# Kernel tuning notes

Hardware: AMD Instinct MI355X
Metric: run time of the kernel (lower is better)

Reference implementation:

```python
import jax, jax.numpy as jnp
import numpy as np

# DeepSeek-V2 router config
T = 8192          # tokens (batch*seq)
H = 5120          # hidden_size / gating_dim
E = 160           # n_routed_experts
N_GROUP = 8       # n_group
TOPK_GROUP = 3    # topk_group
TOP_K = 6         # num_experts_per_tok
SCALE = 16.0      # routed_scaling_factor (norm_topk_prob=False path)


def setup_inputs() -> dict:
    key = jax.random.key(0)
    k1, k2 = jax.random.split(key)
    hidden_states = jax.random.normal(k1, (T, H), dtype=jnp.float32)
    # kaiming_uniform init for the gating kernel
    bound = float(np.sqrt(6.0 / H))
    kernel = jax.random.uniform(k2, (E, H), dtype=jnp.float32, minval=-bound, maxval=bound)
    return {"hidden_states": hidden_states, "kernel": kernel}


def reference(hidden_states, kernel):
    # gating matmul in fp32: [T, H] @ [H, E] -> [T, E]
    logits = jnp.einsum("th,eh->te", hidden_states.astype(jnp.float32), kernel.astype(jnp.float32))
    scores = jax.nn.softmax(logits, axis=-1)  # [T, E]

    n_tok = scores.shape[0]
    # group-limited greedy: max score per group -> [T, N_GROUP]
    group_scores = scores.reshape(n_tok, N_GROUP, E // N_GROUP).max(axis=-1)
    top_group_idx = jax.lax.top_k(group_scores, TOPK_GROUP)[1]  # [T, TOPK_GROUP]

    # scatter 1s into selected groups
    row_idx = jnp.arange(n_tok)[:, None]
    group_mask = jnp.zeros_like(group_scores).at[row_idx, top_group_idx].set(1.0)  # [T, N_GROUP]

    # broadcast group mask over experts within each group -> [T, E]
    score_mask = jnp.repeat(group_mask[:, :, None], E // N_GROUP, axis=2).reshape(n_tok, -1)
    masked_scores = jnp.where(score_mask, scores, 0.0)

    topk_weight, _ = jax.lax.top_k(masked_scores, TOP_K)  # [T, TOP_K]
    # norm_topk_prob is False in DeepSeek-V2 -> scale by routed_scaling_factor
    return topk_weight * SCALE
```

## Files before the change

### kernel.cpp

```cpp
#include <hip/hip_runtime.h>
#include <math.h>

#define TT 8192
#define HH 5120
#define EE 160
#define NGRP 8
#define GSZ 20
#define TOPKG 3
#define TOPK 6
#define RSCALE 16.0f
#define SK 8
#define KS (HH / SK)
#define NSG (KS / 32)
#define BMG 256

typedef __attribute__((ext_vector_type(8))) short bf16x8;
typedef __attribute__((ext_vector_type(8))) _Float16 f16x8;
typedef __attribute__((ext_vector_type(4))) float f32x4;

#define BW_ELEMS ((size_t)160 * 10 * 64 * 8)
#define BWH_BYTES (BW_ELEMS * 2)

__device__ __forceinline__ ushort f2bf(float f) {
    uint32_t u = __float_as_uint(f);
    u += 0x7fff + ((u >> 16) & 1);
    return (ushort)(u >> 16);
}
__device__ __forceinline__ float bf2f(ushort h) {
    return __uint_as_float(((uint32_t)h) << 16);
}

__device__ __forceinline__ f16x8 cvt8(f32x4 x, f32x4 y) {
    f16x8 r;
    r[0] = (_Float16)x[0]; r[1] = (_Float16)x[1];
    r[2] = (_Float16)x[2]; r[3] = (_Float16)x[3];
    r[4] = (_Float16)y[0]; r[5] = (_Float16)y[1];
    r[6] = (_Float16)y[2]; r[7] = (_Float16)y[3];
    return r;
}

__global__ __launch_bounds__(256) void prep_b_f16(const float* __restrict__ B,
                                                  ushort* __restrict__ Bw) {
    int gid = blockIdx.x * 256 + threadIdx.x;
    int lane = gid & 63;
    int et   = (gid >> 6) % 10;
    int kt   = gid / 640;
    int e = et * 16 + (lane & 15);
    int c = kt * 32 + (lane >> 4) * 8;
    const float* src = B + (size_t)e * HH + c;
    f32x4 s0 = *(const f32x4*)src;
    f32x4 s1 = *(const f32x4*)(src + 4);
    union { f16x8 h; uint4 v; } u;
    u.h = cvt8(s0, s1);
    *reinterpret_cast<uint4*>(Bw + (size_t)gid * 8) = u.v;
}

__global__ __launch_bounds__(512, 2) void moe_gemm(const float* __restrict__ A,
                                                   const ushort* __restrict__ Bw,
                                                   float* __restrict__ P) {
    __shared__ char lds[2][10240];

    const int tid = threadIdx.x;
    const int w = tid >> 6, l = tid & 63;
    const int mb  = blockIdx.x & 31;
    const int ks  = blockIdx.x >> 5;
    const int bm0 = mb * BMG;
    const int kt0 = ks * NSG;

    const int row = l & 15, koct = l >> 4;

    const float* apA = A + (size_t)(bm0 + 32 * w + row) * HH + ks * KS + koct * 8;
    const float* apB = apA + (size_t)16 * HH;

    const char* BwB = (const char*)Bw;
    const int u0 = tid, u1 = tid + 512;

    f32x4 acc[2][10];
    #pragma unroll
    for (int i = 0; i < 2; i++)
        #pragma unroll
        for (int et = 0; et < 10; et++) acc[i][et] = (f32x4){0.f, 0.f, 0.f, 0.f};

    uint4 r0, r1;
    {
        size_t tb = (size_t)kt0 * 10240;
        r0 = *(const uint4*)(BwB + tb + (size_t)u0 * 16);
        if (tid < 128) r1 = *(const uint4*)(BwB + tb + (size_t)u1 * 16);
    }
    f32x4 pa0 = *(const f32x4*)(apA), pa1 = *(const f32x4*)(apA + 4);
    f32x4 pa2 = *(const f32x4*)(apB), pa3 = *(const f32x4*)(apB + 4);
    *(uint4*)(lds[0] + u0 * 16) = r0;
    if (tid < 128) *(uint4*)(lds[0] + u1 * 16) = r1;
    __syncthreads();

    #pragma unroll 1
    for (int s = 0; s < NSG; ++s) {
        const int cur = s & 1;
        const bool more = (s + 1 < NSG);
        uint4 n0, n1;
        f32x4 na0 = pa0, na1 = pa1, na2 = pa2, na3 = pa3;
        if (more) {
            size_t tb = (size_t)(kt0 + s + 1) * 10240;
            n0 = *(const uint4*)(BwB + tb + (size_t)u0 * 16);
            if (tid < 128) n1 = *(const uint4*)(BwB + tb + (size_t)u1 * 16);
            const float* a = apA + (s + 1) * 32;
            const float* b = apB + (s + 1) * 32;
            na0 = *(const f32x4*)(a); na1 = *(const f32x4*)(a + 4);
            na2 = *(const f32x4*)(b); na3 = *(const f32x4*)(b + 4);
        }

        f16x8 ah0 = cvt8(pa0, pa1);
        f16x8 ah1 = cvt8(pa2, pa3);

        const char* LB = lds[cur];
        #pragma unroll
        for (int et = 0; et < 10; ++et) {
            f16x8 bh = *(const f16x8*)(LB + et * 1024 + l * 16);
            acc[0][et] = __builtin_amdgcn_mfma_f32_16x16x32_f16(ah0, bh, acc[0][et], 0, 0, 0);
            acc[1][et] = __builtin_amdgcn_mfma_f32_16x16x32_f16(ah1, bh, acc[1][et], 0, 0, 0);
        }
        __syncthreads();
        if (more) {
            char* LN = lds[1 - cur];
            *(uint4*)(LN + u0 * 16) = n0;
            if (tid < 128) *(uint4*)(LN + u1 * 16) = n1;
        }
        pa0 = na0; pa1 = na1; pa2 = na2; pa3 = na3;
        __syncthreads();
    }

    const int rrow = koct * 4;
    #pragma unroll
    for (int i = 0; i < 2; i++)
        #pragma unroll
        for (int et = 0; et < 10; et++)
            #pragma unroll
            for (int j = 0; j < 4; j++)
                P[((size_t)ks * TT + bm0 + 32 * w + 16 * i + rrow + j) * EE + et * 16 + row]
                    = acc[i][et][j];
}

__global__ __launch_bounds__(512, 4) void moe_route(const float* __restrict__ P,
                                                    float* __restrict__ out) {
    const int w = threadIdx.x >> 6, l = threadIdx.x & 63;
    const int t = blockIdx.x * 8 + w;

    float s0 = 0.f, s1 = 0.f, s2 = 0.f;
    #pragma unroll
    for (int sl = 0; sl < SK; ++sl) {
        const float* b = P + ((size_t)sl * TT + t) * EE;
        s0 += b[l];
        s1 += b[64 + l];
        if (l < 32) s2 += b[128 + l];
    }
    if (l >= 32) s2 = -INFINITY;

    float m = fmaxf(s0, fmaxf(s1, s2));
    #pragma unroll
    for (int off = 32; off >= 1; off >>= 1) m = fmaxf(m, __shfl_xor(m, off, 64));
    float p0 = expf(s0 - m);
    float p1 = expf(s1 - m);
    float p2 = (l < 32) ? expf(s2 - m) : 0.f;
    float sum = p0 + p1 + p2;
    #pragma unroll
    for (int off = 32; off >= 1; off >>= 1) sum += __shfl_xor(sum, off, 64);
    float inv = 1.0f / sum;
    p0 *= inv; p1 *= inv; p2 *= inv;

    const int g0 = l / GSZ;
    const int g1 = (l + 64) / GSZ;
    const int g2 = (l + 128) / GSZ;

    float gmax[NGRP];
    #pragma unroll
    for (int g = 0; g < NGRP; g++) {
        float v = -1.f;
        if (g0 == g) v = p0;
        if (g1 == g) v = fmaxf(v, p1);
        if (l < 32 && g2 == g) v = fmaxf(v, p2);
        #pragma unroll
        for (int off = 32; off >= 1; off >>= 1) v = fmaxf(v, __shfl_xor(v, off, 64));
        gmax[g] = v;
    }

    int selmask = 0;
    #pragma unroll
    for (int s = 0; s < TOPKG; s++) {
        float best = -2.f; int bg = 0;
        #pragma unroll
        for (int g = 0; g < NGRP; g++)
            if (!((selmask >> g) & 1) && gmax[g] > best) { best = gmax[g]; bg = g; }
        selmask |= 1 << bg;
    }

    float m0 = ((selmask >> g0) & 1) ? p0 : 0.f;
    float m1 = ((selmask >> g1) & 1) ? p1 : 0.f;
    float m2 = (l < 32) ? (((selmask >> g2) & 1) ? p2 : 0.f) : -1.f;

    #pragma unroll
    for (int s = 0; s < TOPK; s++) {
        float v = fmaxf(m0, fmaxf(m1, m2));
        #pragma unroll
        for (int off = 32; off >= 1; off >>= 1) v = fmaxf(v, __shfl_xor(v, off, 64));
        int idx = 0x7fffffff;
        if (m0 == v) idx = l;
        if (m1 == v) idx = min(idx, l + 64);
        if (l < 32 && m2 == v) idx = min(idx, l + 128);
        #pragma unroll
        for (int off = 32; off >= 1; off >>= 1) idx = min(idx, __shfl_xor(idx, off, 64));
        if (idx == l)            m0 = -1.f;
        else if (idx == l + 64)  m1 = -1.f;
        else if (l < 32 && idx == l + 128) m2 = -1.f;
        if (l == 0) out[(size_t)t * TOPK + s] = v * RSCALE;
    }
}

#define BM 16
#define KW 640
#define NS (KW / 32)
#define PS (EE + 1)

__global__ __launch_bounds__(256) void prep_b_bf16(const float* __restrict__ B,
                                                   ushort* __restrict__ Bw) {
    int gid = blockIdx.x * 256 + threadIdx.x;
    int lane = gid & 63;
    int et   = (gid >> 6) % 10;
    int kt   = gid / 640;
    int e = et * 16 + (lane & 15);
    int c = kt * 32 + (lane >> 4) * 8;
    const float* src = B + (size_t)e * HH + c;
    uint4 vh, vl;
    uint32_t hw[8], lw[8];
    #pragma unroll
    for (int j = 0; j < 8; j++) {
        float f = src[j];
        ushort h = f2bf(f);
        float r = f - bf2f(h);
        hw[j] = h;
        lw[j] = f2bf(r);
    }
    vh.x = hw[0] | (hw[1] << 16); vh.y = hw[2] | (hw[3] << 16);
    vh.z = hw[4] | (hw[5] << 16); vh.w = hw[6] | (hw[7] << 16);
    vl.x = lw[0] | (lw[1] << 16); vl.y = lw[2] | (lw[3] << 16);
    vl.z = lw[4] | (lw[5] << 16); vl.w = lw[6] | (lw[7] << 16);
    *reinterpret_cast<uint4*>(Bw + (size_t)gid * 8) = vh;
    *reinterpret_cast<uint4*>(Bw + BW_ELEMS + (size_t)gid * 8) = vl;
}

__device__ __forceinline__ void split8(f32x4 x, f32x4 y, bf16x8& ah, bf16x8& al) {
    float fv[8] = {x[0], x[1], x[2], x[3], y[0], y[1], y[2], y[3]};
    union { uint32_t u[4]; bf16x8 v; } H, L;
    #pragma unroll
    for (int j = 0; j < 4; j++) {
        ushort h0 = f2bf(fv[2*j]), h1 = f2bf(fv[2*j+1]);
        float  r0 = fv[2*j]   - bf2f(h0);
        float  r1 = fv[2*j+1] - bf2f(h1);
        H.u[j] = (uint32_t)h0 | ((uint32_t)h1 << 16);
        L.u[j] = (uint32_t)f2bf(r0) | ((uint32_t)f2bf(r1) << 16);
    }
    ah = H.v; al = L.v;
}

__global__ __launch_bounds__(512, 4) void moe_mfma(const float* __restrict__ A,
                                                   const ushort* __restrict__ Bw,
                                                   float* __restrict__ out) {
    __shared__ float Sc[BM * PS];

    const int tid = threadIdx.x;
    const int w = tid >> 6, l = tid & 63;
    const int bm0 = blockIdx.x * BM;
    const int row  = l & 15;
    const int koct = l >> 4;

    f32x4 acc[10];
    #pragma unroll
    for (int et = 0; et < 10; et++) acc[et] = (f32x4){0.f, 0.f, 0.f, 0.f};

    const float* apw = A + (size_t)(bm0 + row) * HH + w * KW + koct * 8;

    #pragma unroll 1
    for (int s = 0; s < NS; ++s) {
        const f32x4* p = (const f32x4*)(apw + s * 32);
        bf16x8 ah, al;
        split8(p[0], p[1], ah, al);
        const ushort* bt = Bw + ((size_t)((w * NS + s) * 10) * 64 + (size_t)l) * 8;
        #pragma unroll
        for (int et = 0; et < 10; ++et) {
            bf16x8 bh = *(const bf16x8*)(bt + et * 512);
            bf16x8 bl = *(const bf16x8*)(bt + BW_ELEMS + et * 512);
            acc[et] = __builtin_amdgcn_mfma_f32_16x16x32_bf16(ah, bh, acc[et], 0, 0, 0);
            acc[et] = __builtin_amdgcn_mfma_f32_16x16x32_bf16(al, bh, acc[et], 0, 0, 0);
            acc[et] = __builtin_amdgcn_mfma_f32_16x16x32_bf16(ah, bl, acc[et], 0, 0, 0);
        }
    }

    for (int i = tid; i < BM * PS; i += 512) Sc[i] = 0.f;
    __syncthreads();
    const int rrow = koct * 4;
    #pragma unroll
    for (int et = 0; et < 10; et++)
        #pragma unroll
        for (int j = 0; j < 4; j++)
            atomicAdd(&Sc[(rrow + j) * PS + et * 16 + row], acc[et][j]);
    __syncthreads();

    for (int it = 0; it < 2; ++it) {
        const int r = w * 2 + it;
        float s0 = Sc[r * PS + l];
        float s1 = Sc[r * PS + 64 + l];
        float s2 = (l < 32) ? Sc[r * PS + 128 + l] : -INFINITY;

        float m = fmaxf(s0, fmaxf(s1, s2));
        #pragma unroll
        for (int off = 32; off >= 1; off >>= 1) m = fmaxf(m, __shfl_xor(m, off, 64));
        float p0 = expf(s0 - m);
        float p1 = expf(s1 - m);
        float p2 = (l < 32) ? expf(s2 - m) : 0.f;
        float sum = p0 + p1 + p2;
        #pragma unroll
        for (int off = 32; off >= 1; off >>= 1) sum += __shfl_xor(sum, off, 64);
        float inv = 1.0f / sum;
        p0 *= inv; p1 *= inv; p2 *= inv;

        const int g0 = l / GSZ;
        const int g1 = (l + 64) / GSZ;
        const int g2 = (l + 128) / GSZ;

        float gmax[NGRP];
        #pragma unroll
        for (int g = 0; g < NGRP; g++) {
            float v = -1.f;
            if (g0 == g) v = p0;
            if (g1 == g) v = fmaxf(v, p1);
            if (l < 32 && g2 == g) v = fmaxf(v, p2);
            #pragma unroll
            for (int off = 32; off >= 1; off >>= 1) v = fmaxf(v, __shfl_xor(v, off, 64));
            gmax[g] = v;
        }

        int selmask = 0;
        #pragma unroll
        for (int s = 0; s < TOPKG; s++) {
            float best = -2.f; int bg = 0;
            #pragma unroll
            for (int g = 0; g < NGRP; g++)
                if (!((selmask >> g) & 1) && gmax[g] > best) { best = gmax[g]; bg = g; }
            selmask |= 1 << bg;
        }

        float m0 = ((selmask >> g0) & 1) ? p0 : 0.f;
        float m1 = ((selmask >> g1) & 1) ? p1 : 0.f;
        float m2 = (l < 32) ? (((selmask >> g2) & 1) ? p2 : 0.f) : -1.f;

        #pragma unroll
        for (int s = 0; s < TOPK; s++) {
            float v = fmaxf(m0, fmaxf(m1, m2));
            #pragma unroll
            for (int off = 32; off >= 1; off >>= 1) v = fmaxf(v, __shfl_xor(v, off, 64));
            int idx = 0x7fffffff;
            if (m0 == v) idx = l;
            if (m1 == v) idx = min(idx, l + 64);
            if (l < 32 && m2 == v) idx = min(idx, l + 128);
            #pragma unroll
            for (int off = 32; off >= 1; off >>= 1) idx = min(idx, __shfl_xor(idx, off, 64));
            if (idx == l)            m0 = -1.f;
            else if (idx == l + 64)  m1 = -1.f;
            else if (l < 32 && idx == l + 128) m2 = -1.f;
            if (l == 0) out[(size_t)(bm0 + r) * TOPK + s] = v * RSCALE;
        }
    }
}

extern "C" void kernel_launch(void* const* d_in, const int* in_sizes, int n_in,
                              void* d_out, int out_size, void* d_ws, size_t ws_size,
                              hipStream_t stream) {
    const float* hs = (const float*)d_in[0];
    const float* kn = (const float*)d_in[1];
    float* o = (float*)d_out;

    const size_t pBytes = (size_t)SK * TT * EE * 4;
    if (ws_size >= BWH_BYTES + pBytes) {
        ushort* Bw = (ushort*)d_ws;
        float*  P  = (float*)((char*)d_ws + BWH_BYTES);
        hipLaunchKernelGGL(prep_b_f16, dim3(400),     dim3(256), 0, stream, kn, Bw);
        hipLaunchKernelGGL(moe_gemm,   dim3(32 * SK), dim3(512), 0, stream, hs, Bw, P);
        hipLaunchKernelGGL(moe_route,  dim3(TT / 8),  dim3(512), 0, stream, P, o);
    } else {
        ushort* Bw = (ushort*)d_ws;
        hipLaunchKernelGGL(prep_b_bf16, dim3(400),    dim3(256), 0, stream, kn, Bw);
        hipLaunchKernelGGL(moe_mfma,   dim3(TT / BM), dim3(512), 0, stream, hs, Bw, o);
    }
}
```

Baseline: 63.19 us.

## Halve split-K and M tile, one A fragment per warp, drop mid-loop barrier

Split-K drops from 8 to 4 slices and the M tile shrinks from 256 to 128 rows, so each warp now handles 16 rows with one A fragment instead of two. The grid keeps the same block count. The partial-sum buffer that the routing kernel reads is halved, which cuts the write and read traffic between the two kernels. The barrier between the MFMA loop and the store into the next LDS buffer is removed, which the double buffering still keeps safe. In exchange, each staged B tile now feeds half as many MFMAs and each block reads twice as much of B.

```diff
diff --git a/kernel.cpp b/kernel.cpp
--- a/kernel.cpp
+++ b/kernel.cpp
@@ -9,10 +9,10 @@
 #define TOPKG 3
 #define TOPK 6
 #define RSCALE 16.0f
-#define SK 8
+#define SK 4
 #define KS (HH / SK)
 #define NSG (KS / 32)
-#define BMG 256
+#define BMG 128
 
 typedef __attribute__((ext_vector_type(8))) short bf16x8;
 typedef __attribute__((ext_vector_type(8))) _Float16 f16x8;
@@ -62,82 +62,73 @@
 
     const int tid = threadIdx.x;
     const int w = tid >> 6, l = tid & 63;
-    const int mb  = blockIdx.x & 31;
-    const int ks  = blockIdx.x >> 5;
+    const int mb  = blockIdx.x & 63;
+    const int ks  = blockIdx.x >> 6;
     const int bm0 = mb * BMG;
     const int kt0 = ks * NSG;
 
     const int row = l & 15, koct = l >> 4;
 
-    const float* apA = A + (size_t)(bm0 + 32 * w + row) * HH + ks * KS + koct * 8;
-    const float* apB = apA + (size_t)16 * HH;
+    const float* apA = A + (size_t)(bm0 + 16 * w + row) * HH + ks * KS + koct * 8;
 
     const char* BwB = (const char*)Bw;
     const int u0 = tid, u1 = tid + 512;
 
-    f32x4 acc[2][10];
-    #pragma unroll
-    for (int i = 0; i < 2; i++)
-        #pragma unroll
-        for (int et = 0; et < 10; et++) acc[i][et] = (f32x4){0.f, 0.f, 0.f, 0.f};
-
-    uint4 r0, r1;
+    f32x4 acc[10];
+    #pragma unroll
+    for (int et = 0; et < 10; et++) acc[et] = (f32x4){0.f, 0.f, 0.f, 0.f};
+
     {
         size_t tb = (size_t)kt0 * 10240;
-        r0 = *(const uint4*)(BwB + tb + (size_t)u0 * 16);
-        if (tid < 128) r1 = *(const uint4*)(BwB + tb + (size_t)u1 * 16);
+        uint4 r0 = *(const uint4*)(BwB + tb + (size_t)u0 * 16);
+        *(uint4*)(lds[0] + u0 * 16) = r0;
+        if (tid < 128) {
+            uint4 r1 = *(const uint4*)(BwB + tb + (size_t)u1 * 16);
+            *(uint4*)(lds[0] + u1 * 16) = r1;
+        }
     }
     f32x4 pa0 = *(const f32x4*)(apA), pa1 = *(const f32x4*)(apA + 4);
-    f32x4 pa2 = *(const f32x4*)(apB), pa3 = *(const f32x4*)(apB + 4);
-    *(uint4*)(lds[0] + u0 * 16) = r0;
-    if (tid < 128) *(uint4*)(lds[0] + u1 * 16) = r1;
     __syncthreads();
 
     #pragma unroll 1
     for (int s = 0; s < NSG; ++s) {
         const int cur = s & 1;
         const bool more = (s + 1 < NSG);
+
         uint4 n0, n1;
-        f32x4 na0 = pa0, na1 = pa1, na2 = pa2, na3 = pa3;
+        f32x4 na0 = pa0, na1 = pa1;
         if (more) {
             size_t tb = (size_t)(kt0 + s + 1) * 10240;
             n0 = *(const uint4*)(BwB + tb + (size_t)u0 * 16);
             if (tid < 128) n1 = *(const uint4*)(BwB + tb + (size_t)u1 * 16);
             const float* a = apA + (s + 1) * 32;
-            const float* b = apB + (s + 1) * 32;
             na0 = *(const f32x4*)(a); na1 = *(const f32x4*)(a + 4);
-            na2 = *(const f32x4*)(b); na3 = *(const f32x4*)(b + 4);
-        }
-
-        f16x8 ah0 = cvt8(pa0, pa1);
-        f16x8 ah1 = cvt8(pa2, pa3);
-
+        }
+
+        f16x8 a16 = cvt8(pa0, pa1);
         const char* LB = lds[cur];
         #pragma unroll
         for (int et = 0; et < 10; ++et) {
             f16x8 bh = *(const f16x8*)(LB + et * 1024 + l * 16);
-            acc[0][et] = __builtin_amdgcn_mfma_f32_16x16x32_f16(ah0, bh, acc[0][et], 0, 0, 0);
-            acc[1][et] = __builtin_amdgcn_mfma_f32_16x16x32_f16(ah1, bh, acc[1][et], 0, 0, 0);
-        }
-        __syncthreads();
+            acc[et] = __builtin_amdgcn_mfma_f32_16x16x32_f16(a16, bh, acc[et], 0, 0, 0);
+        }
+
         if (more) {
             char* LN = lds[1 - cur];
             *(uint4*)(LN + u0 * 16) = n0;
             if (tid < 128) *(uint4*)(LN + u1 * 16) = n1;
         }
-        pa0 = na0; pa1 = na1; pa2 = na2; pa3 = na3;
+        pa0 = na0; pa1 = na1;
         __syncthreads();
     }
 
     const int rrow = koct * 4;
     #pragma unroll
-    for (int i = 0; i < 2; i++)
-        #pragma unroll
-        for (int et = 0; et < 10; et++)
-            #pragma unroll
-            for (int j = 0; j < 4; j++)
-                P[((size_t)ks * TT + bm0 + 32 * w + 16 * i + rrow + j) * EE + et * 16 + row]
-                    = acc[i][et][j];
+    for (int et = 0; et < 10; et++)
+        #pragma unroll
+        for (int j = 0; j < 4; j++)
+            P[((size_t)ks * TT + bm0 + 16 * w + rrow + j) * EE + et * 16 + row]
+                = acc[et][j];
 }
 
 __global__ __launch_bounds__(512, 4) void moe_route(const float* __restrict__ P,
@@ -383,7 +374,7 @@
         ushort* Bw = (ushort*)d_ws;
         float*  P  = (float*)((char*)d_ws + BWH_BYTES);
         hipLaunchKernelGGL(prep_b_f16, dim3(400),     dim3(256), 0, stream, kn, Bw);
-        hipLaunchKernelGGL(moe_gemm,   dim3(32 * SK), dim3(512), 0, stream, hs, Bw, P);
+        hipLaunchKernelGGL(moe_gemm,   dim3(64 * SK), dim3(512), 0, stream, hs, Bw, P);
         hipLaunchKernelGGL(moe_route,  dim3(TT / 8),  dim3(512), 0, stream, P, o);
     } else {
         ushort* Bw = (ushort*)d_ws;
```

New measurement: 65.24 us. +3.2%, slower.
